# Kernel optimization log

Measured on AMD Instinct MI355X. Metric: run time of the kernel, lower is better.

The kernel has to match this reference:

```python
import jax, jax.numpy as jnp
import numpy as np

B, N, H = 4, 2048, 128
NUM_HEADS = 4
HEAD_DIM = H // NUM_HEADS
SCALE = np.sqrt(HEAD_DIM).astype(np.float32)


def setup_inputs() -> dict:
    key = jax.random.key(0)
    ks = jax.random.split(key, 16)

    def lin_w(k, o, i):
        return jax.random.normal(k, (o, i), dtype=jnp.float32) / np.sqrt(i).astype(np.float32)

    def lin_b(k, o, i):
        return jax.random.uniform(k, (o,), dtype=jnp.float32, minval=-1, maxval=1) / np.sqrt(i).astype(np.float32)

    return {
        "h": jax.random.normal(ks[0], (B, N, H), dtype=jnp.float32),
        "coords": jax.random.normal(ks[1], (B, N, 3), dtype=jnp.float32),
        "mask": jnp.ones((B, N), dtype=bool),
        "Wq": lin_w(ks[2], H, H), "bq": lin_b(ks[3], H, H),
        "Wk": lin_w(ks[4], H, H), "bk": lin_b(ks[5], H, H),
        "Wv": lin_w(ks[6], H, H), "bv": lin_b(ks[7], H, H),
        "Wo": lin_w(ks[8], H, H), "bo": lin_b(ks[9], H, H),
        "Wc1": lin_w(ks[10], H, H), "bc1": lin_b(ks[11], H, H),
        "Wc2": lin_w(ks[12], 1, H),  # no bias
    }


def reference(h, coords, mask, Wq, bq, Wk, bk, Wv, bv, Wo, bo, Wc1, bc1, Wc2):
    b, n, hd = h.shape
    # projections (torch Linear: y = x @ W.T + b), split heads
    Q = (h @ Wq.T + bq).reshape(b, n, NUM_HEADS, HEAD_DIM)
    K = (h @ Wk.T + bk).reshape(b, n, NUM_HEADS, HEAD_DIM)
    V = (h @ Wv.T + bv).reshape(b, n, NUM_HEADS, HEAD_DIM)

    # scores: (B, heads, N, N)
    scores = jnp.einsum('bnhd,bmhd->bhnm', Q, K) / SCALE
    # mask over keys (last dim), as in torch: mask (B,1,1,N)
    scores = jnp.where(mask[:, None, None, :], scores, -jnp.inf)
    attn = jax.nn.softmax(scores, axis=-1)  # dropout is identity in eval

    h_attn = jnp.einsum('bhnm,bmhd->bnhd', attn, V).reshape(b, n, hd)
    h_out = h_attn @ Wo.T + bo

    # scalar gate per node, softmax over nodes (dim=1)
    cw = jax.nn.silu(h @ Wc1.T + bc1) @ Wc2.T  # (B, N, 1)
    cw = jax.nn.softmax(cw, axis=1)

    # coords_update[b,n] = sum_m a[n,m]*(coords[n]-coords[m])
    #                    = (sum_m a[n,m]) * coords[n] - A @ coords
    # (avoids materializing the B x N x N x 3 coords_diff tensor; same math)
    attn_mean = attn.mean(axis=1)  # (B, N, N)
    row_sum = attn_mean.sum(axis=-1, keepdims=True)  # (B, N, 1)
    coords_update = row_sum * coords - jnp.einsum('bnm,bmd->bnd', attn_mean, coords)
    coords_out = coords + coords_update * cw
    return h_out, coords_out
```

## Files before the change

### kernel.cpp

```cpp
#include <hip/hip_runtime.h>
#include <hip/hip_bf16.h>


typedef __bf16    bf16x8 __attribute__((ext_vector_type(8)));
typedef __bf16    bf16x4 __attribute__((ext_vector_type(4)));
typedef _Float16  f16x8  __attribute__((ext_vector_type(8)));
typedef _Float16  f16x4  __attribute__((ext_vector_type(4)));
typedef float     f32x4  __attribute__((ext_vector_type(4)));

constexpr float QK_E2 = 0.2550316861118708f;

__device__ inline float fast_exp2(float x) {
#if __has_builtin(__builtin_amdgcn_exp2f)
    return __builtin_amdgcn_exp2f(x);
#else
    return exp2f(x);
#endif
}

__device__ inline bf16x8 cvt8(const float* p) {
    float4 a = *(const float4*)p;
    float4 b = *(const float4*)(p + 4);
    bf16x8 o;
    o[0] = (__bf16)a.x; o[1] = (__bf16)a.y; o[2] = (__bf16)a.z; o[3] = (__bf16)a.w;
    o[4] = (__bf16)b.x; o[5] = (__bf16)b.y; o[6] = (__bf16)b.z; o[7] = (__bf16)b.w;
    return o;
}

__global__ __launch_bounds__(256) void prep(
    const float* __restrict__ coords,
    const float* __restrict__ Wq, const float* __restrict__ Wk,
    const float* __restrict__ Wv, const float* __restrict__ Wc1,
    const float* __restrict__ Wo,
    __hip_bfloat16* __restrict__ Wsw, _Float16* __restrict__ Csw)
{
    const int tid = threadIdx.x, blk = blockIdx.x;
    if (blk < 40) {
        int lin = blk * 256 + tid;
        int lane = lin & 63, rest = lin >> 6;
        int sub = rest & 7, mk = rest >> 3;
        int mat = mk >> 2, k4 = mk & 3;
        int col = lane & 15, quad = lane >> 4;
        const float* W = (mat == 0) ? Wq : (mat == 1) ? Wk :
                         (mat == 2) ? Wv : (mat == 3) ? Wc1 : Wo;
        bf16x8 o = cvt8(W + (size_t)(sub * 16 + col) * 128 + k4 * 32 + quad * 8);
        *(bf16x8*)(Wsw + (size_t)lin * 8) = o;
    } else {
        int lin = (blk - 40) * 256 + tid;
        int lane = lin & 63, bk2 = lin >> 6;
        int col = lane & 15, quad = lane >> 4;
        f16x4 o;
        if (col < 3) {
            #pragma unroll
            for (int j = 0; j < 4; ++j)
                o[j] = (_Float16)coords[((size_t)bk2 * 16 + quad * 4 + j) * 3 + col];
        } else if (col == 3) {
            o[0] = o[1] = o[2] = o[3] = (_Float16)1.f;
        } else {
            o[0] = o[1] = o[2] = o[3] = (_Float16)0.f;
        }
        *(f16x4*)(Csw + (size_t)lin * 4) = o;
    }
}

__global__ __launch_bounds__(256) void proj_mfma(
    const float* __restrict__ h, const __hip_bfloat16* __restrict__ Wsw,
    const float* __restrict__ bq, const float* __restrict__ bk,
    const float* __restrict__ bv, const float* __restrict__ bc1,
    const float* __restrict__ Wc2,
    __hip_bfloat16* __restrict__ Qb, __hip_bfloat16* __restrict__ Kb,
    _Float16* __restrict__ Vsw, float* __restrict__ g)
{
    __shared__ float sh[16 * 132];

    const int tid = threadIdx.x;
    const int wave = tid >> 6, lane = tid & 63;
    const int col = lane & 15, quad = lane >> 4;
    const int row0 = blockIdx.x * 16;
    const int b = row0 >> 11, n0 = row0 & 2047;

    {
        int idx = tid * 8, r = idx >> 7, c0 = idx & 127;
        float4 v0 = *(const float4*)(h + (size_t)(row0 + r) * 128 + c0);
        float4 v1 = *(const float4*)(h + (size_t)(row0 + r) * 128 + c0 + 4);
        *(float4*)(sh + r * 132 + c0) = v0;
        *(float4*)(sh + r * 132 + c0 + 4) = v1;
    }
    __syncthreads();

    bf16x8 a[4];
    #pragma unroll
    for (int k4 = 0; k4 < 4; ++k4)
        a[k4] = cvt8(sh + col * 132 + k4 * 32 + quad * 8);

    f32x4 acc[8];
    #pragma unroll
    for (int s = 0; s < 8; ++s) acc[s] = (f32x4){0.f, 0.f, 0.f, 0.f};

    #pragma unroll
    for (int k4 = 0; k4 < 4; ++k4) {
        #pragma unroll
        for (int sub = 0; sub < 8; ++sub) {
            bf16x8 bf = *(const bf16x8*)(Wsw +
                (((size_t)(wave * 4 + k4) * 8 + sub) * 64 + lane) * 8);
            acc[sub] = __builtin_amdgcn_mfma_f32_16x16x32_bf16(a[k4], bf, acc[sub], 0, 0, 0);
        }
    }

    if (wave == 0) {
        #pragma unroll
        for (int sub = 0; sub < 8; ++sub) {
            int c = sub * 16 + col, head = c >> 5, d = c & 31;
            float bias = bq[c];
            size_t base = (size_t)(b * 4 + head) * 2048 + n0 + quad * 4;
            #pragma unroll
            for (int r = 0; r < 4; ++r)
                Qb[(base + r) * 32 + d] = __float2bfloat16((acc[sub][r] + bias) * QK_E2);
        }
    } else if (wave == 1) {
        #pragma unroll
        for (int sub = 0; sub < 8; ++sub) {
            int c = sub * 16 + col, head = c >> 5, d = c & 31;
            float bias = bk[c];
            size_t base = (size_t)(b * 4 + head) * 2048 + n0 + quad * 4;
            #pragma unroll
            for (int r = 0; r < 4; ++r)
                Kb[(base + r) * 32 + d] = __float2bfloat16(acc[sub][r] + bias);
        }
    } else if (wave == 2) {
        const int kc = n0 >> 4;
        #pragma unroll
        for (int sub = 0; sub < 8; ++sub) {
            int c = sub * 16 + col, head = c >> 5;
            float bias = bv[c];
            f16x4 vv;
            #pragma unroll
            for (int r = 0; r < 4; ++r) vv[r] = (_Float16)(acc[sub][r] + bias);
            *(f16x4*)(Vsw + (((size_t)(b * 4 + head) * 128 + kc) * 64
                             + quad * 16 + col) * 8 + (sub & 1) * 4) = vv;
        }
    } else {
        float gsum[4] = {0.f, 0.f, 0.f, 0.f};
        #pragma unroll
        for (int sub = 0; sub < 8; ++sub) {
            int c = sub * 16 + col;
            float bias = bc1[c], w2 = Wc2[c];
            #pragma unroll
            for (int r = 0; r < 4; ++r) {
                float x = acc[sub][r] + bias;
                gsum[r] += (x / (1.f + __expf(-x))) * w2;
            }
        }
        #pragma unroll
        for (int r = 0; r < 4; ++r) {
            gsum[r] += __shfl_xor(gsum[r], 1);
            gsum[r] += __shfl_xor(gsum[r], 2);
            gsum[r] += __shfl_xor(gsum[r], 4);
            gsum[r] += __shfl_xor(gsum[r], 8);
            if (col == 0) g[row0 + quad * 4 + r] = gsum[r];
        }
    }
}

__global__ __launch_bounds__(256, 4) void attn_mfma(
    const __hip_bfloat16* __restrict__ Qb, const __hip_bfloat16* __restrict__ Kb,
    const _Float16* __restrict__ Vsw, const _Float16* __restrict__ Csw,
    __hip_bfloat16* __restrict__ hsw, float* __restrict__ Ach)
{
    __shared__ f32x4 red[6][4][64];

    const int tid = threadIdx.x;
    const int wave = tid >> 6, lane = tid & 63;
    const int col = lane & 15, quad = lane >> 4;

    const int bid = blockIdx.x;
    const int xcd = bid & 7, slot = bid >> 3;
    const int bh = xcd * 2 + (slot >> 6);
    const int q0 = (slot & 63) * 32;
    const int b = bh >> 2;

    const __hip_bfloat16* Qp = Qb + ((size_t)bh * 2048 + q0) * 32;
    const bf16x8 qA = *(const bf16x8*)(Qp + (size_t)col * 32 + quad * 8);
    const bf16x8 qB = *(const bf16x8*)(Qp + (size_t)(16 + col) * 32 + quad * 8);

    const __hip_bfloat16* Kp = Kb + ((size_t)bh * 2048 + wave * 512) * 32;
    const _Float16* Vp = Vsw + ((size_t)bh * 128 + wave * 32) * 512;
    const _Float16* Cp = Csw + ((size_t)b * 128 + wave * 32) * 256;

    f32x4 oLoA = {0,0,0,0}, oHiA = {0,0,0,0}, cA = {0,0,0,0};
    f32x4 oLoB = {0,0,0,0}, oHiB = {0,0,0,0}, cB = {0,0,0,0};
    const f32x4 fz = {0,0,0,0};

    bf16x8 kbuf[4]; f16x8 vbuf[4]; f16x4 cbuf[4];
    #pragma unroll
    for (int s = 0; s < 3; ++s) {
        kbuf[s] = *(const bf16x8*)(Kp + (size_t)(s * 16 + col) * 32 + quad * 8);
        vbuf[s] = *(const f16x8*)(Vp + (size_t)s * 512 + lane * 8);
        cbuf[s] = *(const f16x4*)(Cp + (size_t)s * 256 + lane * 4);
    }

    #pragma unroll 4
    for (int it = 0; it < 32; ++it) {
        const int pf = (it + 3 < 32) ? (it + 3) : 31;
        const int ws2 = (it + 3) & 3;
        kbuf[ws2] = *(const bf16x8*)(Kp + (size_t)(pf * 16 + col) * 32 + quad * 8);
        vbuf[ws2] = *(const f16x8*)(Vp + (size_t)pf * 512 + lane * 8);
        cbuf[ws2] = *(const f16x4*)(Cp + (size_t)pf * 256 + lane * 4);

        const int rs = it & 3;
        bf16x8 kf = kbuf[rs];
        f16x8 v8  = vbuf[rs];
        f16x4 cf  = cbuf[rs];

        f32x4 sA = __builtin_amdgcn_mfma_f32_16x16x32_bf16(kf, qA, fz, 0, 0, 0);
        f32x4 sB = __builtin_amdgcn_mfma_f32_16x16x32_bf16(kf, qB, fz, 0, 0, 0);

        f16x4 pA, pB;
        #pragma unroll
        for (int r = 0; r < 4; ++r) {
            pA[r] = (_Float16)fast_exp2(sA[r]);
            pB[r] = (_Float16)fast_exp2(sB[r]);
        }

        f16x4 vlo = {v8[0], v8[1], v8[2], v8[3]};
        f16x4 vhi = {v8[4], v8[5], v8[6], v8[7]};

        oLoA = __builtin_amdgcn_mfma_f32_16x16x16f16(vlo, pA, oLoA, 0, 0, 0);
        oHiA = __builtin_amdgcn_mfma_f32_16x16x16f16(vhi, pA, oHiA, 0, 0, 0);
        cA   = __builtin_amdgcn_mfma_f32_16x16x16f16(cf,  pA, cA,   0, 0, 0);
        oLoB = __builtin_amdgcn_mfma_f32_16x16x16f16(vlo, pB, oLoB, 0, 0, 0);
        oHiB = __builtin_amdgcn_mfma_f32_16x16x16f16(vhi, pB, oHiB, 0, 0, 0);
        cB   = __builtin_amdgcn_mfma_f32_16x16x16f16(cf,  pB, cB,   0, 0, 0);
    }

    red[0][wave][lane] = oLoA; red[1][wave][lane] = oHiA; red[2][wave][lane] = cA;
    red[3][wave][lane] = oLoB; red[4][wave][lane] = oHiB; red[5][wave][lane] = cB;
    __syncthreads();
    if (wave >= 2) return;

    const int base = wave * 3;
    f32x4 oLo = red[base+0][0][lane], oHi = red[base+1][0][lane], cc = red[base+2][0][lane];
    #pragma unroll
    for (int w = 1; w < 4; ++w) {
        oLo += red[base+0][w][lane];
        oHi += red[base+1][w][lane];
        cc  += red[base+2][w][lane];
    }
    float l = red[base+2][0][col][3] + red[base+2][1][col][3] +
              red[base+2][2][col][3] + red[base+2][3][col][3];
    float invl = 1.f / l;

    const int t = (b * 2048 + q0) / 16 + wave;
    bf16x4 lo4, hi4;
    #pragma unroll
    for (int r = 0; r < 4; ++r) {
        lo4[r] = (__bf16)(oLo[r] * invl);
        hi4[r] = (__bf16)(oHi[r] * invl);
    }
    const int head = bh & 3;
    *(bf16x4*)(hsw + ((size_t)(t * 4 + head) * 64 + (quad >> 1) * 16 + col) * 8
                    + (quad & 1) * 4) = lo4;
    *(bf16x4*)(hsw + ((size_t)(t * 4 + head) * 64 + (2 + (quad >> 1)) * 16 + col) * 8
                    + (quad & 1) * 4) = hi4;

    if (quad == 0) {
        const int q = q0 + wave * 16 + col;
        #pragma unroll
        for (int r = 0; r < 3; ++r)
            Ach[((size_t)bh * 2048 + q) * 3 + r] = cc[r] * invl;
    }
}

__global__ __launch_bounds__(256) void out_mfma(
    const __hip_bfloat16* __restrict__ hsw, const __hip_bfloat16* __restrict__ Wsw,
    const float* __restrict__ bo, const float* __restrict__ coords,
    const float* __restrict__ Ach, const float* __restrict__ g,
    float* __restrict__ out_h, float* __restrict__ out_c)
{
    __shared__ float sred[8];

    const int tid = threadIdx.x;
    const int wave = tid >> 6, lane = tid & 63;
    const int col = lane & 15, quad = lane >> 4;
    const int t = blockIdx.x, row0 = t * 16;
    const int b = row0 >> 11;
    const float* gb = g + (size_t)b * 2048;

    float4 g0 = *(const float4*)(gb + tid * 8);
    float4 g1 = *(const float4*)(gb + tid * 8 + 4);
    float mx = fmaxf(fmaxf(fmaxf(g0.x, g0.y), fmaxf(g0.z, g0.w)),
                     fmaxf(fmaxf(g1.x, g1.y), fmaxf(g1.z, g1.w)));
    #pragma unroll
    for (int off = 32; off; off >>= 1) mx = fmaxf(mx, __shfl_xor(mx, off));
    if (lane == 0) sred[wave] = mx;
    __syncthreads();
    float M = fmaxf(fmaxf(sred[0], sred[1]), fmaxf(sred[2], sred[3]));
    float sum = __expf(g0.x - M) + __expf(g0.y - M) + __expf(g0.z - M) + __expf(g0.w - M)
              + __expf(g1.x - M) + __expf(g1.y - M) + __expf(g1.z - M) + __expf(g1.w - M);
    #pragma unroll
    for (int off = 32; off; off >>= 1) sum += __shfl_xor(sum, off);
    if (lane == 0) sred[4 + wave] = sum;
    __syncthreads();
    float invS = 1.f / (sred[4] + sred[5] + sred[6] + sred[7]);

    bf16x8 a[4];
    #pragma unroll
    for (int k4 = 0; k4 < 4; ++k4)
        a[k4] = *(const bf16x8*)(hsw + ((size_t)(t * 4 + k4) * 64 + lane) * 8);

    f32x4 acc[2] = {{0.f,0.f,0.f,0.f}, {0.f,0.f,0.f,0.f}};
    #pragma unroll
    for (int k4 = 0; k4 < 4; ++k4) {
        #pragma unroll
        for (int sub = 0; sub < 2; ++sub) {
            int c16 = wave * 2 + sub;
            bf16x8 bf = *(const bf16x8*)(Wsw +
                (((size_t)(16 + k4) * 8 + c16) * 64 + lane) * 8);
            acc[sub] = __builtin_amdgcn_mfma_f32_16x16x32_bf16(a[k4], bf, acc[sub], 0, 0, 0);
        }
    }

    #pragma unroll
    for (int sub = 0; sub < 2; ++sub) {
        int c = (wave * 2 + sub) * 16 + col;
        float bias = bo[c];
        #pragma unroll
        for (int r = 0; r < 4; ++r)
            out_h[(size_t)(row0 + quad * 4 + r) * 128 + c] = acc[sub][r] + bias;
    }

    if (tid < 48) {
        int r = tid / 3, d2 = tid % 3;
        size_t row = (size_t)row0 + r;
        int nloc = (int)(row & 2047);
        float am = 0.f;
        #pragma unroll
        for (int hh = 0; hh < 4; ++hh)
            am += Ach[((size_t)(b * 4 + hh) * 2048 + nloc) * 3 + d2];
        am *= 0.25f;
        float cwv = __expf(gb[nloc] - M) * invS;
        float c = coords[row * 3 + d2];
        out_c[row * 3 + d2] = c + (c - am) * cwv;
    }
}

extern "C" void kernel_launch(void* const* d_in, const int* in_sizes, int n_in,
                              void* d_out, int out_size, void* d_ws, size_t ws_size,
                              hipStream_t stream)
{
    (void)in_sizes; (void)n_in; (void)out_size; (void)ws_size;

    const float* h      = (const float*)d_in[0];
    const float* coords = (const float*)d_in[1];
    const float* Wq  = (const float*)d_in[3];  const float* bq  = (const float*)d_in[4];
    const float* Wk  = (const float*)d_in[5];  const float* bk  = (const float*)d_in[6];
    const float* Wv  = (const float*)d_in[7];  const float* bv  = (const float*)d_in[8];
    const float* Wo  = (const float*)d_in[9];  const float* bo  = (const float*)d_in[10];
    const float* Wc1 = (const float*)d_in[11]; const float* bc1 = (const float*)d_in[12];
    const float* Wc2 = (const float*)d_in[13];

    __hip_bfloat16* Qb   = (__hip_bfloat16*)d_ws;
    __hip_bfloat16* Kb   = Qb + 1048576;
    __hip_bfloat16* hsw  = Kb + 1048576;
    __hip_bfloat16* Wsw  = hsw + 1048576;
    _Float16* Vsw = (_Float16*)(Wsw + 81920);
    _Float16* Csw = Vsw + 1048576;
    float* fp  = (float*)(Csw + 131072);
    float* g   = fp;
    float* Ach = fp + 8192;

    float* out_h = (float*)d_out;
    float* out_c = out_h + (size_t)4 * 2048 * 128;

    hipLaunchKernelGGL(prep, dim3(168), dim3(256), 0, stream,
                       coords, Wq, Wk, Wv, Wc1, Wo, Wsw, Csw);
    hipLaunchKernelGGL(proj_mfma, dim3(512), dim3(256), 0, stream,
                       h, Wsw, bq, bk, bv, bc1, Wc2, Qb, Kb, Vsw, g);
    hipLaunchKernelGGL(attn_mfma, dim3(1024), dim3(256), 0, stream,
                       Qb, Kb, Vsw, Csw, hsw, Ach);
    hipLaunchKernelGGL(out_mfma, dim3(512), dim3(256), 0, stream,
                       hsw, Wsw, bo, coords, Ach, g, out_h, out_c);
}
```

Before: 112.8 us.

## Fuse attention and output projection into one kernel with all heads per block

```diff
diff --git a/kernel.cpp b/kernel.cpp
--- a/kernel.cpp
+++ b/kernel.cpp
@@ -162,12 +162,17 @@
     }
 }
 
-__global__ __launch_bounds__(256, 4) void attn_mfma(
+__global__ __launch_bounds__(512, 2) void attn_out(
     const __hip_bfloat16* __restrict__ Qb, const __hip_bfloat16* __restrict__ Kb,
     const _Float16* __restrict__ Vsw, const _Float16* __restrict__ Csw,
-    __hip_bfloat16* __restrict__ hsw, float* __restrict__ Ach)
+    const __hip_bfloat16* __restrict__ Wsw, const float* __restrict__ g,
+    const float* __restrict__ coords, const float* __restrict__ bo,
+    float* __restrict__ out_h, float* __restrict__ out_c)
 {
-    __shared__ f32x4 red[6][4][64];
+    __shared__ f32x4 red[6][8][64];
+    __shared__ __bf16 hsw_s[2][4][64][8];
+    __shared__ float ach_s[2][16][4][3];
+    __shared__ float gsred[16];
 
     const int tid = threadIdx.x;
     const int wave = tid >> 6, lane = tid & 63;
@@ -175,17 +180,39 @@
 
     const int bid = blockIdx.x;
     const int xcd = bid & 7, slot = bid >> 3;
-    const int bh = xcd * 2 + (slot >> 6);
-    const int q0 = (slot & 63) * 32;
-    const int b = bh >> 2;
+    const int b = xcd >> 1;
+    const int q0 = ((xcd & 1) * 32 + slot) * 32;
+    const int head = wave >> 1, half = wave & 1;
+    const int bh = b * 4 + head;
+
+    const float* gb = g + (size_t)b * 2048;
+    float4 gv = *(const float4*)(gb + tid * 4);
+    float mx = fmaxf(fmaxf(gv.x, gv.y), fmaxf(gv.z, gv.w));
+    #pragma unroll
+    for (int off = 32; off; off >>= 1) mx = fmaxf(mx, __shfl_xor(mx, off));
+    if (lane == 0) gsred[wave] = mx;
+    __syncthreads();
+    float M = gsred[0];
+    #pragma unroll
+    for (int w = 1; w < 8; ++w) M = fmaxf(M, gsred[w]);
+    float sum = __expf(gv.x - M) + __expf(gv.y - M)
+              + __expf(gv.z - M) + __expf(gv.w - M);
+    #pragma unroll
+    for (int off = 32; off; off >>= 1) sum += __shfl_xor(sum, off);
+    if (lane == 0) gsred[8 + wave] = sum;
+    __syncthreads();
+    float ssum = gsred[8];
+    #pragma unroll
+    for (int w = 9; w < 16; ++w) ssum += gsred[w];
+    const float invS = 1.f / ssum;
 
     const __hip_bfloat16* Qp = Qb + ((size_t)bh * 2048 + q0) * 32;
     const bf16x8 qA = *(const bf16x8*)(Qp + (size_t)col * 32 + quad * 8);
     const bf16x8 qB = *(const bf16x8*)(Qp + (size_t)(16 + col) * 32 + quad * 8);
 
-    const __hip_bfloat16* Kp = Kb + ((size_t)bh * 2048 + wave * 512) * 32;
-    const _Float16* Vp = Vsw + ((size_t)bh * 128 + wave * 32) * 512;
-    const _Float16* Cp = Csw + ((size_t)b * 128 + wave * 32) * 256;
+    const __hip_bfloat16* Kp = Kb + ((size_t)bh * 2048 + half * 1024) * 32;
+    const _Float16* Vp = Vsw + ((size_t)bh * 128 + half * 64) * 512;
+    const _Float16* Cp = Csw + ((size_t)b * 128 + half * 64) * 256;
 
     f32x4 oLoA = {0,0,0,0}, oHiA = {0,0,0,0}, cA = {0,0,0,0};
     f32x4 oLoB = {0,0,0,0}, oHiB = {0,0,0,0}, cB = {0,0,0,0};
@@ -200,8 +227,8 @@
     }
 
     #pragma unroll 4
-    for (int it = 0; it < 32; ++it) {
-        const int pf = (it + 3 < 32) ? (it + 3) : 31;
+    for (int it = 0; it < 64; ++it) {
+        const int pf = (it + 3 < 64) ? (it + 3) : 63;
         const int ws2 = (it + 3) & 3;
         kbuf[ws2] = *(const bf16x8*)(Kp + (size_t)(pf * 16 + col) * 32 + quad * 8);
         vbuf[ws2] = *(const f16x8*)(Vp + (size_t)pf * 512 + lane * 8);
@@ -236,109 +263,71 @@
     red[0][wave][lane] = oLoA; red[1][wave][lane] = oHiA; red[2][wave][lane] = cA;
     red[3][wave][lane] = oLoB; red[4][wave][lane] = oHiB; red[5][wave][lane] = cB;
     __syncthreads();
-    if (wave >= 2) return;
-
-    const int base = wave * 3;
-    f32x4 oLo = red[base+0][0][lane], oHi = red[base+1][0][lane], cc = red[base+2][0][lane];
-    #pragma unroll
-    for (int w = 1; w < 4; ++w) {
-        oLo += red[base+0][w][lane];
-        oHi += red[base+1][w][lane];
-        cc  += red[base+2][w][lane];
-    }
-    float l = red[base+2][0][col][3] + red[base+2][1][col][3] +
-              red[base+2][2][col][3] + red[base+2][3][col][3];
-    float invl = 1.f / l;
-
-    const int t = (b * 2048 + q0) / 16 + wave;
-    bf16x4 lo4, hi4;
-    #pragma unroll
-    for (int r = 0; r < 4; ++r) {
-        lo4[r] = (__bf16)(oLo[r] * invl);
-        hi4[r] = (__bf16)(oHi[r] * invl);
-    }
-    const int head = bh & 3;
-    *(bf16x4*)(hsw + ((size_t)(t * 4 + head) * 64 + (quad >> 1) * 16 + col) * 8
-                    + (quad & 1) * 4) = lo4;
-    *(bf16x4*)(hsw + ((size_t)(t * 4 + head) * 64 + (2 + (quad >> 1)) * 16 + col) * 8
-                    + (quad & 1) * 4) = hi4;
-
-    if (quad == 0) {
-        const int q = q0 + wave * 16 + col;
-        #pragma unroll
-        for (int r = 0; r < 3; ++r)
-            Ach[((size_t)bh * 2048 + q) * 3 + r] = cc[r] * invl;
-    }
-}
-
-__global__ __launch_bounds__(256) void out_mfma(
-    const __hip_bfloat16* __restrict__ hsw, const __hip_bfloat16* __restrict__ Wsw,
-    const float* __restrict__ bo, const float* __restrict__ coords,
-    const float* __restrict__ Ach, const float* __restrict__ g,
-    float* __restrict__ out_h, float* __restrict__ out_c)
-{
-    __shared__ float sred[8];
-
-    const int tid = threadIdx.x;
-    const int wave = tid >> 6, lane = tid & 63;
-    const int col = lane & 15, quad = lane >> 4;
-    const int t = blockIdx.x, row0 = t * 16;
-    const int b = row0 >> 11;
-    const float* gb = g + (size_t)b * 2048;
-
-    float4 g0 = *(const float4*)(gb + tid * 8);
-    float4 g1 = *(const float4*)(gb + tid * 8 + 4);
-    float mx = fmaxf(fmaxf(fmaxf(g0.x, g0.y), fmaxf(g0.z, g0.w)),
-                     fmaxf(fmaxf(g1.x, g1.y), fmaxf(g1.z, g1.w)));
-    #pragma unroll
-    for (int off = 32; off; off >>= 1) mx = fmaxf(mx, __shfl_xor(mx, off));
-    if (lane == 0) sred[wave] = mx;
-    __syncthreads();
-    float M = fmaxf(fmaxf(sred[0], sred[1]), fmaxf(sred[2], sred[3]));
-    float sum = __expf(g0.x - M) + __expf(g0.y - M) + __expf(g0.z - M) + __expf(g0.w - M)
-              + __expf(g1.x - M) + __expf(g1.y - M) + __expf(g1.z - M) + __expf(g1.w - M);
-    #pragma unroll
-    for (int off = 32; off; off >>= 1) sum += __shfl_xor(sum, off);
-    if (lane == 0) sred[4 + wave] = sum;
-    __syncthreads();
-    float invS = 1.f / (sred[4] + sred[5] + sred[6] + sred[7]);
-
-    bf16x8 a[4];
-    #pragma unroll
-    for (int k4 = 0; k4 < 4; ++k4)
-        a[k4] = *(const bf16x8*)(hsw + ((size_t)(t * 4 + k4) * 64 + lane) * 8);
-
-    f32x4 acc[2] = {{0.f,0.f,0.f,0.f}, {0.f,0.f,0.f,0.f}};
-    #pragma unroll
-    for (int k4 = 0; k4 < 4; ++k4) {
+
+    {
+        const int h = wave >> 1, gq = wave & 1;
+        const int base = gq * 3;
+        const int w0 = h * 2, w1 = h * 2 + 1;
+        f32x4 oLo = red[base+0][w0][lane] + red[base+0][w1][lane];
+        f32x4 oHi = red[base+1][w0][lane] + red[base+1][w1][lane];
+        f32x4 cc  = red[base+2][w0][lane] + red[base+2][w1][lane];
+        float l = red[base+2][w0][col][3] + red[base+2][w1][col][3];
+        float invl = 1.f / l;
+
+        bf16x4 lo4, hi4;
+        #pragma unroll
+        for (int r = 0; r < 4; ++r) {
+            lo4[r] = (__bf16)(oLo[r] * invl);
+            hi4[r] = (__bf16)(oHi[r] * invl);
+        }
+        *(bf16x4*)(&hsw_s[gq][h][(quad >> 1) * 16 + col][(quad & 1) * 4]) = lo4;
+        *(bf16x4*)(&hsw_s[gq][h][(2 + (quad >> 1)) * 16 + col][(quad & 1) * 4]) = hi4;
+
+        if (quad == 0) {
+            #pragma unroll
+            for (int r = 0; r < 3; ++r)
+                ach_s[gq][col][h][r] = cc[r] * invl;
+        }
+    }
+    __syncthreads();
+
+    {
+        const int tl = wave >> 2, cg = wave & 3;
+        bf16x8 a[4];
+        #pragma unroll
+        for (int k4 = 0; k4 < 4; ++k4)
+            a[k4] = *(const bf16x8*)(&hsw_s[tl][k4][lane][0]);
+
+        f32x4 acc[2] = {{0.f,0.f,0.f,0.f}, {0.f,0.f,0.f,0.f}};
+        #pragma unroll
+        for (int k4 = 0; k4 < 4; ++k4) {
+            #pragma unroll
+            for (int sub = 0; sub < 2; ++sub) {
+                int c16 = cg * 2 + sub;
+                bf16x8 bf = *(const bf16x8*)(Wsw +
+                    (((size_t)(16 + k4) * 8 + c16) * 64 + lane) * 8);
+                acc[sub] = __builtin_amdgcn_mfma_f32_16x16x32_bf16(a[k4], bf, acc[sub], 0, 0, 0);
+            }
+        }
+
+        const size_t row_base = (size_t)b * 2048 + q0 + tl * 16;
         #pragma unroll
         for (int sub = 0; sub < 2; ++sub) {
-            int c16 = wave * 2 + sub;
-            bf16x8 bf = *(const bf16x8*)(Wsw +
-                (((size_t)(16 + k4) * 8 + c16) * 64 + lane) * 8);
-            acc[sub] = __builtin_amdgcn_mfma_f32_16x16x32_bf16(a[k4], bf, acc[sub], 0, 0, 0);
-        }
-    }
-
-    #pragma unroll
-    for (int sub = 0; sub < 2; ++sub) {
-        int c = (wave * 2 + sub) * 16 + col;
-        float bias = bo[c];
-        #pragma unroll
-        for (int r = 0; r < 4; ++r)
-            out_h[(size_t)(row0 + quad * 4 + r) * 128 + c] = acc[sub][r] + bias;
-    }
-
-    if (tid < 48) {
+            int c = (cg * 2 + sub) * 16 + col;
+            float bias = bo[c];
+            #pragma unroll
+            for (int r = 0; r < 4; ++r)
+                out_h[(row_base + quad * 4 + r) * 128 + c] = acc[sub][r] + bias;
+        }
+    }
+
+    if (tid < 96) {
         int r = tid / 3, d2 = tid % 3;
-        size_t row = (size_t)row0 + r;
-        int nloc = (int)(row & 2047);
-        float am = 0.f;
-        #pragma unroll
-        for (int hh = 0; hh < 4; ++hh)
-            am += Ach[((size_t)(b * 4 + hh) * 2048 + nloc) * 3 + d2];
-        am *= 0.25f;
+        int nloc = q0 + r;
+        float am = 0.25f * (ach_s[r >> 4][r & 15][0][d2] + ach_s[r >> 4][r & 15][1][d2]
+                          + ach_s[r >> 4][r & 15][2][d2] + ach_s[r >> 4][r & 15][3][d2]);
         float cwv = __expf(gb[nloc] - M) * invS;
+        size_t row = (size_t)b * 2048 + nloc;
         float c = coords[row * 3 + d2];
         out_c[row * 3 + d2] = c + (c - am) * cwv;
     }
@@ -361,13 +350,10 @@
 
     __hip_bfloat16* Qb   = (__hip_bfloat16*)d_ws;
     __hip_bfloat16* Kb   = Qb + 1048576;
-    __hip_bfloat16* hsw  = Kb + 1048576;
-    __hip_bfloat16* Wsw  = hsw + 1048576;
+    __hip_bfloat16* Wsw  = Kb + 1048576;
     _Float16* Vsw = (_Float16*)(Wsw + 81920);
     _Float16* Csw = Vsw + 1048576;
-    float* fp  = (float*)(Csw + 131072);
-    float* g   = fp;
-    float* Ach = fp + 8192;
+    float* g   = (float*)(Csw + 131072);
 
     float* out_h = (float*)d_out;
     float* out_c = out_h + (size_t)4 * 2048 * 128;
@@ -376,8 +362,6 @@
                        coords, Wq, Wk, Wv, Wc1, Wo, Wsw, Csw);
     hipLaunchKernelGGL(proj_mfma, dim3(512), dim3(256), 0, stream,
                        h, Wsw, bq, bk, bv, bc1, Wc2, Qb, Kb, Vsw, g);
-    hipLaunchKernelGGL(attn_mfma, dim3(1024), dim3(256), 0, stream,
-                       Qb, Kb, Vsw, Csw, hsw, Ach);
-    hipLaunchKernelGGL(out_mfma, dim3(512), dim3(256), 0, stream,
-                       hsw, Wsw, bo, coords, Ach, g, out_h, out_c);
-}
+    hipLaunchKernelGGL(attn_out, dim3(256), dim3(512), 0, stream,
+                       Qb, Kb, Vsw, Csw, Wsw, g, coords, bo, out_h, out_c);
+}
```

New measurement: 109.9 us. 1.03x faster.
